# Kernel tuning notes

Hardware: AMD Instinct MI355X
Metric: run time of the kernel (lower is better)

The kernel has to match this reference:

```python
import jax, jax.numpy as jnp
import numpy as np

T, H, I, E = 512, 2048, 1408, 16
G, TOPK_GROUP, TOP_K = 4, 2, 6
RSF = 2.5  # routed_scaling_factor


def setup_inputs() -> dict:
    key = jax.random.key(0)
    ks = jax.random.split(key, 6)
    s = jnp.float32(0.02)
    return {
        "hidden_states": jax.random.normal(ks[0], (T, H), jnp.float32),
        "gate_weight": jax.random.normal(ks[1], (E, H), jnp.float32) * s,
        "correction_bias": jax.random.normal(ks[2], (E,), jnp.float32) * s,
        "w_gate": jax.random.normal(ks[3], (E, I, H), jnp.float32) * s,
        "w_up": jax.random.normal(ks[4], (E, I, H), jnp.float32) * s,
        "w_down": jax.random.normal(ks[5], (E, H, I), jnp.float32) * s,
    }


def _route(x, gate_weight, correction_bias):
    # MoEGate: logits = x @ W^T ; noaux_tc biased grouped top-k (sigmoid scoring)
    logits = x @ gate_weight.T                       # [T, E]
    scores = jax.nn.sigmoid(logits)                  # [T, E]
    sfc = scores + correction_bias                   # scores used for selection only
    # group score = sum of top-2 biased scores within each group
    gs = sfc.reshape(-1, G, E // G)                  # [T, G, E/G]
    group_scores = jax.lax.top_k(gs, 2)[0].sum(-1)   # [T, G]
    gidx = jax.lax.top_k(group_scores, TOPK_GROUP)[1]        # [T, topk_group]
    gmask = jnp.sum(jax.nn.one_hot(gidx, G, dtype=x.dtype), axis=1)  # [T, G]
    emask = jnp.repeat(gmask, E // G, axis=1)        # [T, E]
    masked = jnp.where(emask > 0, sfc, -jnp.inf)
    topk_idx = jax.lax.top_k(masked, TOP_K)[1]       # [T, K]
    # weights come from the UNbiased sigmoid scores
    topk_w = jnp.take_along_axis(scores, topk_idx, axis=1)   # [T, K]
    topk_w = topk_w / jnp.sum(topk_w, axis=-1, keepdims=True)  # renormalize
    topk_w = topk_w * jnp.asarray(RSF, x.dtype)      # routed_scaling_factor
    return topk_w, topk_idx


def _moe(x, topk_w, topk_idx, w_gate, w_up, w_down):
    # dispatch/grouped-GEMM/combine, expressed as a scan over experts with
    # per-token combine coefficients (same math as gather/grouped-GEMM/scatter)
    def step(acc, ws):
        wg, wu, wd, e = ws
        h = jax.nn.silu(x @ wg.T) * (x @ wu.T)       # [T, I] SiluAndMul
        out_e = h @ wd.T                             # [T, H]
        coef = jnp.sum(jnp.where(topk_idx == e, topk_w, 0.0), axis=1)  # [T]
        return acc + coef[:, None] * out_e, None

    acc0 = jnp.zeros_like(x)
    acc, _ = jax.lax.scan(step, acc0, (w_gate, w_up, w_down, jnp.arange(E)))
    return acc


def reference(hidden_states, gate_weight, correction_bias, w_gate, w_up, w_down):
    topk_w, topk_idx = _route(hidden_states, gate_weight, correction_bias)
    return _moe(hidden_states, topk_w, topk_idx, w_gate, w_up, w_down)
```

## Files before the change

### kernel.cpp

```cpp
#include <hip/hip_runtime.h>
#include <cstdint>

#define T_TOK 512
#define H_DIM 2048
#define I_DIM 1408
#define N_EXP 16

typedef __attribute__((ext_vector_type(8))) _Float16 f16x8;
typedef __attribute__((ext_vector_type(4))) float f32x4;

__device__ __forceinline__ void gload_lds16(const void* g, void* l) {
  auto gp = (const __attribute__((address_space(1))) unsigned int*)(unsigned long long)g;
  unsigned int loff = (unsigned int)(unsigned long long)l;
  auto lp = (__attribute__((address_space(3))) unsigned int*)loff;
  __builtin_amdgcn_global_load_lds(gp, lp, 16, 0, 0);
}

__device__ __forceinline__ f16x8 cvt8(f32x4 a, f32x4 b) {
  f16x8 r;
  r[0] = (_Float16)a[0]; r[1] = (_Float16)a[1]; r[2] = (_Float16)a[2]; r[3] = (_Float16)a[3];
  r[4] = (_Float16)b[0]; r[5] = (_Float16)b[1]; r[6] = (_Float16)b[2]; r[7] = (_Float16)b[3];
  return r;
}

__global__ __launch_bounds__(256) void route_kernel(
    const float* __restrict__ x, const float* __restrict__ gw,
    const float* __restrict__ bias, float* __restrict__ coef,
    _Float16* __restrict__ xb) {
  const int t = blockIdx.x;
  const int tid = threadIdx.x;
  const float* xt = x + (size_t)t * H_DIM;
  _Float16* xbt = xb + (size_t)t * H_DIM;

  float part[N_EXP];
#pragma unroll
  for (int e = 0; e < N_EXP; ++e) part[e] = 0.f;
  for (int j = tid; j < H_DIM; j += 256) {
    float xv = xt[j];
    xbt[j] = (_Float16)xv;
#pragma unroll
    for (int e = 0; e < N_EXP; ++e) part[e] += xv * gw[e * H_DIM + j];
  }
#pragma unroll
  for (int e = 0; e < N_EXP; ++e) {
#pragma unroll
    for (int off = 32; off > 0; off >>= 1) part[e] += __shfl_down(part[e], off);
  }
  __shared__ float red[4][N_EXP];
  const int lane = tid & 63, w = tid >> 6;
  if (lane == 0) {
#pragma unroll
    for (int e = 0; e < N_EXP; ++e) red[w][e] = part[e];
  }
  __syncthreads();
  if (tid == 0) {
    float s[16], sf[16];
    for (int e = 0; e < 16; ++e) {
      float lg = red[0][e] + red[1][e] + red[2][e] + red[3][e];
      s[e] = 1.f / (1.f + expf(-lg));
      sf[e] = s[e] + bias[e];
    }
    float gsc[4];
    for (int g = 0; g < 4; ++g) {
      float m1 = -1e30f, m2 = -1e30f;
      for (int j = 0; j < 4; ++j) {
        float v = sf[g * 4 + j];
        if (v > m1) { m2 = m1; m1 = v; }
        else if (v > m2) { m2 = v; }
      }
      gsc[g] = m1 + m2;
    }
    int g1 = 0;
    for (int g = 1; g < 4; ++g) if (gsc[g] > gsc[g1]) g1 = g;
    int g2 = -1;
    for (int g = 0; g < 4; ++g) {
      if (g == g1) continue;
      if (g2 < 0 || gsc[g] > gsc[g2]) g2 = g;
    }
    bool gok[4];
    for (int g = 0; g < 4; ++g) gok[g] = (g == g1) || (g == g2);
    bool sel[16];
    for (int e = 0; e < 16; ++e) sel[e] = false;
    float wsum = 0.f;
    for (int k = 0; k < 6; ++k) {
      int best = -1; float bv = 0.f;
      for (int e2 = 0; e2 < 16; ++e2) {
        if (!gok[e2 >> 2] || sel[e2]) continue;
        if (best < 0 || sf[e2] > bv) { bv = sf[e2]; best = e2; }
      }
      sel[best] = true;
      wsum += s[best];
    }
    float inv = 2.5f / wsum;
    for (int e = 0; e < 16; ++e) coef[t * N_EXP + e] = sel[e] ? s[e] * inv : 0.f;
  }
}

__global__ __launch_bounds__(512) void build_lists_kernel(
    const float* __restrict__ coef, int* __restrict__ counts,
    int* __restrict__ lists) {
  const int e = blockIdx.x;
  const int t = threadIdx.x;
  const bool flag = coef[t * N_EXP + e] != 0.f;
  const unsigned long long m = __ballot(flag);
  const int lane = t & 63, w = t >> 6;
  __shared__ int wcnt[8], woff[8];
  if (lane == 0) wcnt[w] = __popcll(m);
  __syncthreads();
  if (t == 0) {
    int a = 0;
    for (int i = 0; i < 8; ++i) { woff[i] = a; a += wcnt[i]; }
    counts[e] = a;
  }
  __syncthreads();
  if (flag) {
    int pos = woff[w] + __popcll(m & ((1ull << lane) - 1ull));
    lists[e * T_TOK + pos] = t;
  }
}

__global__ __launch_bounds__(256) void gate_up_kernel(
    const _Float16* __restrict__ xb, const float* __restrict__ wg,
    const float* __restrict__ wu, const int* __restrict__ counts,
    const int* __restrict__ lists, _Float16* __restrict__ hbuf) {
  __shared__ char lds[49152];
  const int e = blockIdx.z;
  const int ne = counts[e];
  const int row0 = blockIdx.y * 128;
  if (row0 >= ne) return;
  const int col0 = blockIdx.x * 64;
  const int tid = threadIdx.x;
  const int lane = tid & 63;
  const int w = tid >> 6;
  const int wr = w >> 1, wc = w & 1;

  const int* lst = lists + e * T_TOK;
  const _Float16* asrc[2];
#pragma unroll
  for (int i = 0; i < 2; ++i) {
    int r = row0 + (2 * w + i) * 16 + (lane & 15);
    int tok = lst[min(r, ne - 1)];
    asrc[i] = xb + (size_t)tok * H_DIM + (lane >> 4) * 8;
  }
  const float* bgs[2];
  const float* bus[2];
#pragma unroll
  for (int i = 0; i < 2; ++i) {
    int tr = (w * 2 + i) * 8 + (lane >> 3);
    int ls = (lane & 7) ^ (tr & 7);
    bgs[i] = wg + ((size_t)e * I_DIM + col0 + tr) * H_DIM + ls * 4;
    bus[i] = wu + ((size_t)e * I_DIM + col0 + tr) * H_DIM + ls * 4;
  }

  f32x4 accg[4][2], accu[4][2];
  const f32x4 zz = {0.f, 0.f, 0.f, 0.f};
#pragma unroll
  for (int m = 0; m < 4; ++m)
#pragma unroll
    for (int n = 0; n < 2; ++n) { accg[m][n] = zz; accu[m][n] = zz; }

  auto stage = [&](int kt, int buf) {
    const int k0 = kt * 32;
#pragma unroll
    for (int i = 0; i < 2; ++i)
      gload_lds16(asrc[i] + k0, lds + buf * 8192 + (2 * w + i) * 1024);
#pragma unroll
    for (int i = 0; i < 2; ++i) {
      gload_lds16(bgs[i] + k0, lds + 16384 + buf * 8192 + (w * 2 + i) * 1024);
      gload_lds16(bus[i] + k0, lds + 32768 + buf * 8192 + (w * 2 + i) * 1024);
    }
  };

  auto comp = [&](int buf) {
    const char* Ab = lds + buf * 8192;
    const char* Gb = lds + 16384 + buf * 8192;
    const char* Ub = lds + 32768 + buf * 8192;
    f16x8 afr[4], bg[2], bu[2];
#pragma unroll
    for (int m = 0; m < 4; ++m)
      afr[m] = *(const f16x8*)(Ab + (wr * 4 + m) * 1024 + lane * 16);
    const int s0 = (lane >> 4) * 2;
#pragma unroll
    for (int n = 0; n < 2; ++n) {
      int c = wc * 32 + n * 16 + (lane & 15);
      int p0 = s0 ^ (c & 7);
      int p1 = (s0 + 1) ^ (c & 7);
      bg[n] = cvt8(*(const f32x4*)(Gb + c * 128 + p0 * 16),
                   *(const f32x4*)(Gb + c * 128 + p1 * 16));
      bu[n] = cvt8(*(const f32x4*)(Ub + c * 128 + p0 * 16),
                   *(const f32x4*)(Ub + c * 128 + p1 * 16));
    }
#pragma unroll
    for (int m = 0; m < 4; ++m)
#pragma unroll
      for (int n = 0; n < 2; ++n) {
        accg[m][n] = __builtin_amdgcn_mfma_f32_16x16x32_f16(afr[m], bg[n], accg[m][n], 0, 0, 0);
        accu[m][n] = __builtin_amdgcn_mfma_f32_16x16x32_f16(afr[m], bu[n], accu[m][n], 0, 0, 0);
      }
  };

  const int NK = H_DIM / 32;
  stage(0, 0);
  for (int kt = 0; kt < NK; ++kt) {
    __syncthreads();
    if (kt + 1 < NK) stage(kt + 1, (kt + 1) & 1);
    comp(kt & 1);
  }

  _Float16* hb = hbuf + (size_t)e * T_TOK * I_DIM;
#pragma unroll
  for (int m = 0; m < 4; ++m) {
#pragma unroll
    for (int j = 0; j < 4; ++j) {
      int r = row0 + wr * 64 + m * 16 + (lane >> 4) * 4 + j;
      if (r < ne) {
#pragma unroll
        for (int n = 0; n < 2; ++n) {
          int cc = col0 + wc * 32 + n * 16 + (lane & 15);
          float g = accg[m][n][j];
          float u = accu[m][n][j];
          float hv = (g / (1.f + __expf(-g))) * u;
          hb[(size_t)r * I_DIM + cc] = (_Float16)hv;
        }
      }
    }
  }
}

__global__ __launch_bounds__(512) void down_kernel(
    const _Float16* __restrict__ hbuf, const float* __restrict__ wd,
    const int* __restrict__ counts, const int* __restrict__ lists,
    const float* __restrict__ coef, float* __restrict__ out) {
  extern __shared__ char lds[];
  const int e = blockIdx.z;
  const int ne = counts[e];
  const int row0 = blockIdx.y * 256;
  if (row0 >= ne) return;
  const int col0 = blockIdx.x * 64;
  const int tid = threadIdx.x;
  const int lane = tid & 63;
  const int w = tid >> 6;
  const int wr = w >> 1, wc = w & 1;

  const _Float16* hb = hbuf + (size_t)e * T_TOK * I_DIM;
  const _Float16* asrc[4];
#pragma unroll
  for (int i = 0; i < 4; ++i) {
    int tr = (w * 4 + i) * 8 + (lane >> 3);
    int lchunk = (lane & 7) ^ (tr & 7);
    asrc[i] = hb + (size_t)(row0 + tr) * I_DIM + lchunk * 8;
  }
  const float* bds[2];
#pragma unroll
  for (int i = 0; i < 2; ++i) {
    int tr = (w * 2 + i) * 4 + (lane >> 4);
    int ls = (lane & 15) ^ ((tr & 7) << 1);
    bds[i] = wd + ((size_t)e * H_DIM + col0 + tr) * I_DIM + ls * 4;
  }

  f32x4 acc[4][2];
  const f32x4 zz = {0.f, 0.f, 0.f, 0.f};
#pragma unroll
  for (int m = 0; m < 4; ++m)
#pragma unroll
    for (int n = 0; n < 2; ++n) acc[m][n] = zz;

  auto stage = [&](int kt, int buf) {
    const int k0 = kt * 64;
#pragma unroll
    for (int i = 0; i < 4; ++i)
      gload_lds16(asrc[i] + k0, lds + buf * 32768 + (w * 4 + i) * 1024);
#pragma unroll
    for (int i = 0; i < 2; ++i)
      gload_lds16(bds[i] + k0, lds + 65536 + buf * 16384 + (w * 2 + i) * 1024);
  };

  auto comp = [&](int buf) {
    const char* Ab = lds + buf * 32768;
    const char* Bb = lds + 65536 + buf * 16384;
#pragma unroll
    for (int kk = 0; kk < 2; ++kk) {
      f16x8 afr[4], bf[2];
#pragma unroll
      for (int m = 0; m < 4; ++m) {
        int row = wr * 64 + m * 16 + (lane & 15);
        int pch = (kk * 4 + (lane >> 4)) ^ (row & 7);
        afr[m] = *(const f16x8*)(Ab + row * 128 + pch * 16);
      }
#pragma unroll
      for (int n = 0; n < 2; ++n) {
        int c = wc * 32 + n * 16 + (lane & 15);
        int s0 = kk * 8 + (lane >> 4) * 2;
        int p0 = s0 ^ ((c & 7) << 1);
        int p1 = (s0 + 1) ^ ((c & 7) << 1);
        bf[n] = cvt8(*(const f32x4*)(Bb + c * 256 + p0 * 16),
                     *(const f32x4*)(Bb + c * 256 + p1 * 16));
      }
#pragma unroll
      for (int m = 0; m < 4; ++m)
#pragma unroll
        for (int n = 0; n < 2; ++n)
          acc[m][n] = __builtin_amdgcn_mfma_f32_16x16x32_f16(afr[m], bf[n], acc[m][n], 0, 0, 0);
    }
  };

  const int NK = I_DIM / 64;
  stage(0, 0);
  for (int kt = 0; kt < NK; ++kt) {
    __syncthreads();
    if (kt + 1 < NK) stage(kt + 1, (kt + 1) & 1);
    comp(kt & 1);
  }

#pragma unroll
  for (int m = 0; m < 4; ++m) {
#pragma unroll
    for (int j = 0; j < 4; ++j) {
      int r = row0 + wr * 64 + m * 16 + (lane >> 4) * 4 + j;
      if (r < ne) {
        int tok = lists[e * T_TOK + r];
        float c = coef[tok * N_EXP + e];
#pragma unroll
        for (int n = 0; n < 2; ++n) {
          int cc = col0 + wc * 32 + n * 16 + (lane & 15);
          atomicAdd(&out[(size_t)tok * H_DIM + cc], acc[m][n][j] * c);
        }
      }
    }
  }
}

extern "C" void kernel_launch(void* const* d_in, const int* in_sizes, int n_in,
                              void* d_out, int out_size, void* d_ws, size_t ws_size,
                              hipStream_t stream) {
  const float* x  = (const float*)d_in[0];
  const float* gw = (const float*)d_in[1];
  const float* cb = (const float*)d_in[2];
  const float* wg = (const float*)d_in[3];
  const float* wu = (const float*)d_in[4];
  const float* wd = (const float*)d_in[5];
  float* out = (float*)d_out;
  char* ws = (char*)d_ws;

  float* coef   = (float*)(ws);
  int*   counts = (int*)(ws + 32768);
  int*   lists  = (int*)(ws + 33024);
  _Float16* xb  = (_Float16*)(ws + 66048);
  _Float16* hbuf= (_Float16*)(ws + 66048 + 2097152 + 256);

  hipFuncSetAttribute((const void*)down_kernel,
                      hipFuncAttributeMaxDynamicSharedMemorySize, 98304);

  hipMemsetAsync(d_out, 0, (size_t)out_size * sizeof(float), stream);

  route_kernel<<<T_TOK, 256, 0, stream>>>(x, gw, cb, coef, xb);
  build_lists_kernel<<<N_EXP, 512, 0, stream>>>(coef, counts, lists);
  gate_up_kernel<<<dim3(I_DIM / 64, 4, N_EXP), 256, 0, stream>>>(xb, wg, wu, counts, lists, hbuf);
  down_kernel<<<dim3(H_DIM / 64, 2, N_EXP), 512, 98304, stream>>>(hbuf, wd, counts, lists, coef, out);
}
```

Measured before the change: 245.3 us.

## Retile gate_up so each block covers all expert rows with 32-column weight slices

```diff
diff --git a/kernel.cpp b/kernel.cpp
--- a/kernel.cpp
+++ b/kernel.cpp
@@ -119,38 +119,36 @@
   }
 }
 
-__global__ __launch_bounds__(256) void gate_up_kernel(
+__global__ __launch_bounds__(512, 2) void gate_up_kernel(
     const _Float16* __restrict__ xb, const float* __restrict__ wg,
     const float* __restrict__ wu, const int* __restrict__ counts,
     const int* __restrict__ lists, _Float16* __restrict__ hbuf) {
-  __shared__ char lds[49152];
+  extern __shared__ char lds[];
   const int e = blockIdx.z;
   const int ne = counts[e];
-  const int row0 = blockIdx.y * 128;
-  if (row0 >= ne) return;
-  const int col0 = blockIdx.x * 64;
+  const int col0 = blockIdx.x * 32;
   const int tid = threadIdx.x;
   const int lane = tid & 63;
   const int w = tid >> 6;
-  const int wr = w >> 1, wc = w & 1;
 
   const int* lst = lists + e * T_TOK;
-  const _Float16* asrc[2];
-#pragma unroll
-  for (int i = 0; i < 2; ++i) {
-    int r = row0 + (2 * w + i) * 16 + (lane & 15);
+  const _Float16* asrc[4];
+  bool aact[4];
+#pragma unroll
+  for (int i = 0; i < 4; ++i) {
+    int rbase = w * 64 + i * 16;
+    aact[i] = rbase < ne;
+    int r = rbase + (lane & 15);
     int tok = lst[min(r, ne - 1)];
     asrc[i] = xb + (size_t)tok * H_DIM + (lane >> 4) * 8;
   }
-  const float* bgs[2];
-  const float* bus[2];
-#pragma unroll
-  for (int i = 0; i < 2; ++i) {
-    int tr = (w * 2 + i) * 8 + (lane >> 3);
-    int ls = (lane & 7) ^ (tr & 7);
-    bgs[i] = wg + ((size_t)e * I_DIM + col0 + tr) * H_DIM + ls * 4;
-    bus[i] = wu + ((size_t)e * I_DIM + col0 + tr) * H_DIM + ls * 4;
-  }
+  {
+  }
+  const int btr = (w & 3) * 8 + (lane >> 3);
+  const int bls = (lane & 7) ^ (btr & 7);
+  const float* bsrc = ((w < 4) ? wg : wu) +
+                      ((size_t)e * I_DIM + col0 + btr) * H_DIM + bls * 4;
+  const int bldsoff = (w < 4 ? 65536 : 73728) + (w & 3) * 1024;
 
   f32x4 accg[4][2], accu[4][2];
   const f32x4 zz = {0.f, 0.f, 0.f, 0.f};
@@ -162,27 +160,27 @@
   auto stage = [&](int kt, int buf) {
     const int k0 = kt * 32;
 #pragma unroll
-    for (int i = 0; i < 2; ++i)
-      gload_lds16(asrc[i] + k0, lds + buf * 8192 + (2 * w + i) * 1024);
-#pragma unroll
-    for (int i = 0; i < 2; ++i) {
-      gload_lds16(bgs[i] + k0, lds + 16384 + buf * 8192 + (w * 2 + i) * 1024);
-      gload_lds16(bus[i] + k0, lds + 32768 + buf * 8192 + (w * 2 + i) * 1024);
-    }
+    for (int i = 0; i < 4; ++i)
+      if (aact[i])
+        gload_lds16(asrc[i] + k0, lds + buf * 32768 + (w * 4 + i) * 1024);
+    gload_lds16(bsrc + k0, lds + bldsoff + buf * 4096);
   };
 
+  const bool wact = (w * 64) < ne;
+
   auto comp = [&](int buf) {
-    const char* Ab = lds + buf * 8192;
-    const char* Gb = lds + 16384 + buf * 8192;
-    const char* Ub = lds + 32768 + buf * 8192;
+    if (!wact) return;
+    const char* Ab = lds + buf * 32768;
+    const char* Gb = lds + 65536 + buf * 4096;
+    const char* Ub = lds + 73728 + buf * 4096;
     f16x8 afr[4], bg[2], bu[2];
 #pragma unroll
     for (int m = 0; m < 4; ++m)
-      afr[m] = *(const f16x8*)(Ab + (wr * 4 + m) * 1024 + lane * 16);
+      afr[m] = *(const f16x8*)(Ab + (w * 4 + m) * 1024 + lane * 16);
     const int s0 = (lane >> 4) * 2;
 #pragma unroll
     for (int n = 0; n < 2; ++n) {
-      int c = wc * 32 + n * 16 + (lane & 15);
+      int c = n * 16 + (lane & 15);
       int p0 = s0 ^ (c & 7);
       int p1 = (s0 + 1) ^ (c & 7);
       bg[n] = cvt8(*(const f32x4*)(Gb + c * 128 + p0 * 16),
@@ -207,20 +205,22 @@
     comp(kt & 1);
   }
 
-  _Float16* hb = hbuf + (size_t)e * T_TOK * I_DIM;
-#pragma unroll
-  for (int m = 0; m < 4; ++m) {
-#pragma unroll
-    for (int j = 0; j < 4; ++j) {
-      int r = row0 + wr * 64 + m * 16 + (lane >> 4) * 4 + j;
-      if (r < ne) {
-#pragma unroll
-        for (int n = 0; n < 2; ++n) {
-          int cc = col0 + wc * 32 + n * 16 + (lane & 15);
-          float g = accg[m][n][j];
-          float u = accu[m][n][j];
-          float hv = (g / (1.f + __expf(-g))) * u;
-          hb[(size_t)r * I_DIM + cc] = (_Float16)hv;
+  if (wact) {
+    _Float16* hb = hbuf + (size_t)e * T_TOK * I_DIM;
+#pragma unroll
+    for (int m = 0; m < 4; ++m) {
+#pragma unroll
+      for (int j = 0; j < 4; ++j) {
+        int r = w * 64 + m * 16 + (lane >> 4) * 4 + j;
+        if (r < ne) {
+#pragma unroll
+          for (int n = 0; n < 2; ++n) {
+            int cc = col0 + n * 16 + (lane & 15);
+            float g = accg[m][n][j];
+            float u = accu[m][n][j];
+            float hv = (g / (1.f + __expf(-g))) * u;
+            hb[(size_t)r * I_DIM + cc] = (_Float16)hv;
+          }
         }
       }
     }
@@ -348,6 +348,8 @@
   _Float16* xb  = (_Float16*)(ws + 66048);
   _Float16* hbuf= (_Float16*)(ws + 66048 + 2097152 + 256);
 
+  hipFuncSetAttribute((const void*)gate_up_kernel,
+                      hipFuncAttributeMaxDynamicSharedMemorySize, 81920);
   hipFuncSetAttribute((const void*)down_kernel,
                       hipFuncAttributeMaxDynamicSharedMemorySize, 98304);
 
@@ -355,6 +357,6 @@
 
   route_kernel<<<T_TOK, 256, 0, stream>>>(x, gw, cb, coef, xb);
   build_lists_kernel<<<N_EXP, 512, 0, stream>>>(coef, counts, lists);
-  gate_up_kernel<<<dim3(I_DIM / 64, 4, N_EXP), 256, 0, stream>>>(xb, wg, wu, counts, lists, hbuf);
+  gate_up_kernel<<<dim3(I_DIM / 32, 1, N_EXP), 512, 81920, stream>>>(xb, wg, wu, counts, lists, hbuf);
   down_kernel<<<dim3(H_DIM / 64, 2, N_EXP), 512, 98304, stream>>>(hbuf, wd, counts, lists, coef, out);
 }
```

After: 274.2 us. 11.8% more time.
